# Optimization experiments

Hardware: AMD Instinct MI355X
Metric: run time of the kernel (lower is better)

## Reference

```python
import jax, jax.numpy as jnp
import numpy as np
from jax import lax

INPUT_SIZE = 64
HIDDEN_SIZE = 4096
OUTPUT_SIZE = 16
SEQ_LEN = 4096
SPECTRAL_RADIUS = 0.95
LEAKY_RATE = 0.9
INPUT_SCALING = 1.0
FEEDBACK_SCALING = 0.1
SPARSITY = 0.1


def setup_inputs() -> dict:
    key = jax.random.key(0)
    ks = jax.random.split(key, 7)
    X = jax.random.normal(ks[0], (SEQ_LEN, INPUT_SIZE), dtype=jnp.float32)
    W_in = jax.random.normal(ks[1], (HIDDEN_SIZE, INPUT_SIZE), dtype=jnp.float32) * INPUT_SCALING
    # sparse reservoir matrix, scaled so spectral radius ~ SPECTRAL_RADIUS
    dense = jax.random.normal(ks[2], (HIDDEN_SIZE, HIDDEN_SIZE), dtype=jnp.float32)
    mask = (jax.random.uniform(ks[3], (HIDDEN_SIZE, HIDDEN_SIZE)) < SPARSITY).astype(jnp.float32)
    # circular-law estimate of spectral radius for sparse gaussian: sqrt(density*N)
    scale = SPECTRAL_RADIUS / np.sqrt(SPARSITY * HIDDEN_SIZE)
    W_res = dense * mask * scale
    b = jax.random.normal(ks[4], (HIDDEN_SIZE,), dtype=jnp.float32)
    W_fb = jax.random.normal(ks[5], (HIDDEN_SIZE, OUTPUT_SIZE), dtype=jnp.float32) * FEEDBACK_SCALING
    W_out = jax.random.normal(ks[6], (OUTPUT_SIZE, HIDDEN_SIZE), dtype=jnp.float32) * 0.01
    return {"X": X, "W_in": W_in, "W_res": W_res, "b": b, "W_fb": W_fb, "W_out": W_out}


def reference(X, W_in, W_res, b, W_fb, W_out):
    """ESN with feedback + leaky integration; Force readout (inference: y = W_out @ s).
    Returns (results [T, O], outputs [T, H]) matching ESNForce.forward."""
    H = W_res.shape[0]
    O = W_out.shape[0]

    def step(carry, x_t):
        s, y = carry  # previous state [H], previous output [O]
        pre = W_in @ x_t + W_res @ s + b + W_fb @ y
        s_new = (1.0 - LEAKY_RATE) * s + LEAKY_RATE * jnp.tanh(pre)
        y_new = W_out @ s_new
        return (s_new, y_new), (y_new, s_new)

    init = (jnp.zeros((H,), dtype=X.dtype), jnp.zeros((O,), dtype=X.dtype))
    _, (results, outputs) = lax.scan(step, init, X)
    return results, outputs
```

## Files before the change

### kernel.cpp

```cpp
#include <hip/hip_runtime.h>
#include <cstdint>

#define NBLK 128
#define BLOCK 1024
#define ROWS 32
#define HDIM 4096
#define IDIM 64
#define ODIM 16
#define TSTEPS 4096
#define PAD 576
#define GMAX 18
#define LEAK 0.9f
#define FSTR 16

typedef float f32x4 __attribute__((ext_vector_type(4)));

__global__ void init_ws(unsigned* ws) {
    int i = blockIdx.x * blockDim.x + threadIdx.x;
    if (i < NBLK * FSTR)
        __hip_atomic_store(&ws[i], 0u, __ATOMIC_RELAXED, __HIP_MEMORY_SCOPE_AGENT);
}

__global__ __launch_bounds__(BLOCK) void esn_kernel(
    const float* __restrict__ X,
    const float* __restrict__ Win,
    const float* __restrict__ Wres,
    const float* __restrict__ bvec,
    const float* __restrict__ Wfb,
    const float* __restrict__ Wout,
    float* __restrict__ out,
    float* __restrict__ part,
    unsigned* __restrict__ flags)
{
    __shared__ float          ell_val[ROWS][PAD];
    __shared__ unsigned short ell_idx[ROWS][PAD];
    __shared__ __align__(16) float s_lds[HDIM];
    __shared__ float          win_lds[ROWS][IDIM];
    __shared__ float          wfb_lds[ROWS][ODIM];
    __shared__ __align__(16) float wout_lds[ROWS][ODIM];
    __shared__ float          b_lds[ROWS];
    __shared__ float          x_lds[IDIM];
    __shared__ float          y_lds[ODIM];
    __shared__ __align__(16) float snew_lds[ROWS];
    __shared__ unsigned       prog[NBLK];
    __shared__ int            nnz_lds[ROWS];
    __shared__ int            rnds_lds[ROWS];
    __shared__ unsigned short bankCnt[ROWS][32];
    __shared__ unsigned short grpCnt[ROWS][GMAX];

    const int tid   = threadIdx.x;
    const int blk   = blockIdx.x;
    const int rbase = blk * ROWS;

    for (int i = tid; i < ROWS * PAD; i += BLOCK) {
        ell_val[i / PAD][i % PAD] = 0.0f;
        ell_idx[i / PAD][i % PAD] = 0;
    }
    for (int i = tid; i < ROWS * 32; i += BLOCK) bankCnt[i >> 5][i & 31] = 0;
    for (int i = tid; i < ROWS * GMAX; i += BLOCK) grpCnt[i / GMAX][i % GMAX] = 0;

    {
        const int wave = tid >> 6, lane = tid & 63;
        for (int rr = wave * 2; rr < wave * 2 + 2; ++rr) {
            const float* wrow = Wres + (size_t)(rbase + rr) * HDIM;
            int cnt = 0;
            for (int c0 = 0; c0 < HDIM; c0 += 64)
                cnt += __popcll(__ballot(wrow[c0 + lane] != 0.0f));
            if (lane == 0) {
                int nz = cnt < PAD ? cnt : PAD;
                nnz_lds[rr] = nz;
                int gu = (nz + 31) >> 5;
                if (gu < 1) gu = 1;
                if (gu > GMAX) gu = GMAX;
                rnds_lds[rr] = (gu + 1) >> 1;
            }
        }
    }
    __syncthreads();

    {
        const int wave = tid >> 6, lane = tid & 63;
        if (lane == 0 || lane == 32) {
            const int row = wave * 2 + (lane >> 5);
            const int nz  = nnz_lds[row];
            int gu = (nz + 31) >> 5;
            if (gu < 1) gu = 1;
            if (gu > GMAX) gu = GMAX;
            const float* wrow = Wres + (size_t)(rbase + row) * HDIM;
            int placed = 0;
            for (int c = 0; c < HDIM && placed < nz; ++c) {
                const float w = wrow[c];
                if (w != 0.0f) {
                    const int b = c & 31;
                    const int r = bankCnt[row][b];
                    bankCnt[row][b] = (unsigned short)(r + 1);
                    int g = r % gu;
                    int p = grpCnt[row][g];
                    int guard = 0;
                    while (p >= 32 && guard < GMAX) {
                        g = (g + 1 == gu) ? 0 : g + 1;
                        p = grpCnt[row][g];
                        ++guard;
                    }
                    if (p >= 32) break;
                    grpCnt[row][g] = (unsigned short)(p + 1);
                    const int slot = ((g >> 1) << 6) + 2 * p + (g & 1);
                    ell_val[row][slot] = w;
                    ell_idx[row][slot] = (unsigned short)c;
                    ++placed;
                }
            }
        }
    }

    for (int i = tid; i < ROWS * IDIM; i += BLOCK)
        win_lds[i >> 6][i & 63] = Win[(size_t)(rbase + (i >> 6)) * IDIM + (i & 63)];
    for (int i = tid; i < ROWS * ODIM; i += BLOCK)
        wfb_lds[i >> 4][i & 15] = Wfb[(size_t)(rbase + (i >> 4)) * ODIM + (i & 15)];
    for (int i = tid; i < ROWS * ODIM; i += BLOCK)
        wout_lds[i >> 4][i & 15] = Wout[(size_t)(i & 15) * HDIM + rbase + (i >> 4)];
    if (tid < ROWS) b_lds[tid] = bvec[rbase + tid];

    for (int i = tid; i < HDIM; i += BLOCK) s_lds[i] = 0.0f;
    if (tid < ODIM) y_lds[tid] = 0.0f;
    if (tid >= 64 && tid < 128) x_lds[tid - 64] = X[tid - 64];
    if (tid < NBLK) prog[tid] = 0u;
    __syncthreads();

    float* out_res = out;
    float* out_s   = out + (size_t)TSTEPS * ODIM;

    for (int t = 0; t < TSTEPS; ++t) {
        {
            const int row = tid >> 5;
            const int l   = tid & 31;
            const int R   = rnds_lds[row];
            float a0 = 0.0f, a1 = 0.0f;
            for (int k = 0; k < R; ++k) {
                const int e = (k << 6) + (l << 1);
                const float2  v  = *(const float2*)&ell_val[row][e];
                const ushort2 ix = *(const ushort2*)&ell_idx[row][e];
                a0 += v.x * s_lds[ix.x];
                a1 += v.y * s_lds[ix.y];
            }
            float acc = a0 + a1;
            acc += win_lds[row][l] * x_lds[l] + win_lds[row][l + 32] * x_lds[l + 32];
            if (l < ODIM) acc += wfb_lds[row][l] * y_lds[l];
            acc += __shfl_xor(acc, 16, 32);
            acc += __shfl_xor(acc, 8, 32);
            acc += __shfl_xor(acc, 4, 32);
            acc += __shfl_xor(acc, 2, 32);
            acc += __shfl_xor(acc, 1, 32);
            if (l == 0) {
                const float pre = acc + b_lds[row];
                snew_lds[row] = (1.0f - LEAK) * s_lds[rbase + row] + LEAK * tanhf(pre);
            }
        }
        __syncthreads();

        const int wv = tid >> 6;
        const int ln = tid & 63;
        if (wv == 0) {
            if (ln < ROWS / 4) {
                f32x4 v4 = *(const f32x4*)&snew_lds[ln * 4];
                float* dst = out_s + (size_t)t * HDIM + rbase + ln * 4;
                asm volatile("global_store_dwordx4 %0, %1, off sc0 sc1"
                             :: "v"(dst), "v"(v4) : "memory");
            }
            if (ln < ODIM / 4) {
                f32x4 acc = {0.0f, 0.0f, 0.0f, 0.0f};
                #pragma unroll
                for (int r = 0; r < ROWS; ++r) {
                    f32x4 w = *(const f32x4*)&wout_lds[r][ln * 4];
                    acc += w * snew_lds[r];
                }
                float* dst = part + ((size_t)(t & 1) * NBLK + blk) * ODIM + ln * 4;
                asm volatile("global_store_dwordx4 %0, %1, off sc0 sc1"
                             :: "v"(dst), "v"(acc) : "memory");
            }
            if (ln == 0)
                __hip_atomic_store(&flags[blk * FSTR], (unsigned)(t + 1),
                                   __ATOMIC_RELEASE, __HIP_MEMORY_SCOPE_AGENT);
        } else if (wv == 1) {
            if (t + 1 < TSTEPS) x_lds[ln] = X[(size_t)(t + 1) * IDIM + ln];
            const unsigned tu = (unsigned)(t + 1);
            for (;;) {
                unsigned f0 = __hip_atomic_load(&flags[ln * FSTR],        __ATOMIC_RELAXED, __HIP_MEMORY_SCOPE_AGENT);
                unsigned f1 = __hip_atomic_load(&flags[(ln + 64) * FSTR], __ATOMIC_RELAXED, __HIP_MEMORY_SCOPE_AGENT);
                __hip_atomic_store(&prog[ln],      f0, __ATOMIC_RELAXED, __HIP_MEMORY_SCOPE_WORKGROUP);
                __hip_atomic_store(&prog[ln + 64], f1, __ATOMIC_RELAXED, __HIP_MEMORY_SCOPE_WORKGROUP);
                if (__all(f0 >= tu && f1 >= tu)) break;
                __builtin_amdgcn_s_sleep(1);
            }
            asm volatile("" ::: "memory");
            const int o = ln & 15, j = ln >> 4;
            float* pb = part + (size_t)(t & 1) * NBLK * ODIM;
            float acc = 0.0f;
            #pragma unroll
            for (int k = 0; k < 32; ++k)
                acc += __hip_atomic_load(pb + (size_t)(j + 4 * k) * ODIM + o,
                                         __ATOMIC_RELAXED, __HIP_MEMORY_SCOPE_AGENT);
            acc += __shfl_xor(acc, 16);
            acc += __shfl_xor(acc, 32);
            if (ln < ODIM) {
                if (t + 1 < TSTEPS) y_lds[ln] = acc;
                if (blk == 0) out_res[(size_t)t * ODIM + ln] = acc;
            }
        } else {
            if (t + 1 < TSTEPS) {
                const int wi    = wv - 2;
                const int start = (wi < 2) ? wi * 10 : 20 + (wi - 2) * 9;
                const int count = (wi < 2) ? 10 : 9;
                const unsigned tu = (unsigned)(t + 1);
                for (;;) {
                    unsigned f = (ln < count)
                        ? __hip_atomic_load(&prog[start + ln], __ATOMIC_RELAXED, __HIP_MEMORY_SCOPE_WORKGROUP)
                        : tu;
                    if (__all(f >= tu)) break;
                    __builtin_amdgcn_s_sleep(1);
                }
                asm volatile("" ::: "memory");
                const int c0 = start * ROWS;
                const int n4 = count * (ROWS / 4);
                const float* base = out_s + (size_t)t * HDIM + c0;
                f32x4 v0, v1;
                const float* p0 = base + (size_t)ln * 4;
                asm volatile("global_load_dwordx4 %0, %1, off sc0 sc1"
                             : "=v"(v0) : "v"(p0));
                const bool has2 = (ln + 64) < n4;
                const float* p1 = base + (size_t)(ln + 64) * 4;
                if (has2)
                    asm volatile("global_load_dwordx4 %0, %1, off sc0 sc1"
                                 : "=v"(v1) : "v"(p1));
                asm volatile("s_waitcnt vmcnt(0)" ::: "memory");
                *(f32x4*)&s_lds[c0 + ln * 4] = v0;
                if (has2) *(f32x4*)&s_lds[c0 + (ln + 64) * 4] = v1;
            }
        }
        __syncthreads();
    }
}

extern "C" void kernel_launch(void* const* d_in, const int* in_sizes, int n_in,
                              void* d_out, int out_size, void* d_ws, size_t ws_size,
                              hipStream_t stream) {
    (void)in_sizes; (void)n_in; (void)out_size; (void)ws_size;
    const float* X    = (const float*)d_in[0];
    const float* Win  = (const float*)d_in[1];
    const float* Wres = (const float*)d_in[2];
    const float* b    = (const float*)d_in[3];
    const float* Wfb  = (const float*)d_in[4];
    const float* Wout = (const float*)d_in[5];
    float* out = (float*)d_out;
    unsigned* flags = (unsigned*)d_ws;
    float* part = (float*)d_ws + NBLK * FSTR;

    init_ws<<<8, 256, 0, stream>>>(flags);
    esn_kernel<<<NBLK, BLOCK, 0, stream>>>(X, Win, Wres, b, Wfb, Wout, out, part, flags);
}
```

Before: 21.98 ms.

## Replace flag-based cross-block sync with tagged data packets polled directly

Each 16-byte global store now carries its own step tag, three state values plus a tag or two output partials plus a tag. Consumers poll the data itself until every tag matches, which removes the separate release flag, the LDS progress mirror and the second dependent load round-trip per step. State exchange moves to a double-buffered packed scratch area, and the output partials are split into eight pairs. This relies on 16-byte stores being observed atomically, and busy-polling without sleep raises memory traffic.

```diff
diff --git a/kernel.cpp b/kernel.cpp
--- a/kernel.cpp
+++ b/kernel.cpp
@@ -11,14 +11,15 @@
 #define PAD 576
 #define GMAX 18
 #define LEAK 0.9f
-#define FSTR 16
+#define SU 11
+#define SUS 12
+#define YU 8
 
 typedef float f32x4 __attribute__((ext_vector_type(4)));
 
-__global__ void init_ws(unsigned* ws) {
+__global__ void init_ws(float* ws) {
     int i = blockIdx.x * blockDim.x + threadIdx.x;
-    if (i < NBLK * FSTR)
-        __hip_atomic_store(&ws[i], 0u, __ATOMIC_RELAXED, __HIP_MEMORY_SCOPE_AGENT);
+    if (i < (2 * NBLK * SUS + 2 * NBLK * YU) * 4) ws[i] = 0.0f;
 }
 
 __global__ __launch_bounds__(BLOCK) void esn_kernel(
@@ -29,20 +30,19 @@
     const float* __restrict__ Wfb,
     const float* __restrict__ Wout,
     float* __restrict__ out,
-    float* __restrict__ part,
-    unsigned* __restrict__ flags)
+    float* __restrict__ sx,
+    float* __restrict__ yx)
 {
     __shared__ float          ell_val[ROWS][PAD];
     __shared__ unsigned short ell_idx[ROWS][PAD];
     __shared__ __align__(16) float s_lds[HDIM];
     __shared__ float          win_lds[ROWS][IDIM];
     __shared__ float          wfb_lds[ROWS][ODIM];
-    __shared__ __align__(16) float wout_lds[ROWS][ODIM];
+    __shared__ __align__(8)  float wout_lds[ROWS][ODIM];
     __shared__ float          b_lds[ROWS];
     __shared__ float          x_lds[IDIM];
     __shared__ float          y_lds[ODIM];
     __shared__ __align__(16) float snew_lds[ROWS];
-    __shared__ unsigned       prog[NBLK];
     __shared__ int            nnz_lds[ROWS];
     __shared__ int            rnds_lds[ROWS];
     __shared__ unsigned short bankCnt[ROWS][32];
@@ -124,36 +124,39 @@
     for (int i = tid; i < HDIM; i += BLOCK) s_lds[i] = 0.0f;
     if (tid < ODIM) y_lds[tid] = 0.0f;
     if (tid >= 64 && tid < 128) x_lds[tid - 64] = X[tid - 64];
-    if (tid < NBLK) prog[tid] = 0u;
     __syncthreads();
 
     float* out_res = out;
     float* out_s   = out + (size_t)TSTEPS * ODIM;
 
+    const int rowB = tid >> 5;
+    const int lB   = tid & 31;
+    const int RB   = rnds_lds[rowB];
+
     for (int t = 0; t < TSTEPS; ++t) {
+        const unsigned tu = (unsigned)(t + 1);
+        const float tagf = __uint_as_float(tu);
+
         {
-            const int row = tid >> 5;
-            const int l   = tid & 31;
-            const int R   = rnds_lds[row];
             float a0 = 0.0f, a1 = 0.0f;
-            for (int k = 0; k < R; ++k) {
-                const int e = (k << 6) + (l << 1);
-                const float2  v  = *(const float2*)&ell_val[row][e];
-                const ushort2 ix = *(const ushort2*)&ell_idx[row][e];
+            for (int k = 0; k < RB; ++k) {
+                const int e = (k << 6) + (lB << 1);
+                const float2  v  = *(const float2*)&ell_val[rowB][e];
+                const ushort2 ix = *(const ushort2*)&ell_idx[rowB][e];
                 a0 += v.x * s_lds[ix.x];
                 a1 += v.y * s_lds[ix.y];
             }
             float acc = a0 + a1;
-            acc += win_lds[row][l] * x_lds[l] + win_lds[row][l + 32] * x_lds[l + 32];
-            if (l < ODIM) acc += wfb_lds[row][l] * y_lds[l];
+            acc += win_lds[rowB][lB] * x_lds[lB] + win_lds[rowB][lB + 32] * x_lds[lB + 32];
+            if (lB < ODIM) acc += wfb_lds[rowB][lB] * y_lds[lB];
             acc += __shfl_xor(acc, 16, 32);
             acc += __shfl_xor(acc, 8, 32);
             acc += __shfl_xor(acc, 4, 32);
             acc += __shfl_xor(acc, 2, 32);
             acc += __shfl_xor(acc, 1, 32);
-            if (l == 0) {
-                const float pre = acc + b_lds[row];
-                snew_lds[row] = (1.0f - LEAK) * s_lds[rbase + row] + LEAK * tanhf(pre);
+            if (lB == 0) {
+                const float pre = acc + b_lds[rowB];
+                snew_lds[rowB] = (1.0f - LEAK) * s_lds[rbase + rowB] + LEAK * tanhf(pre);
             }
         }
         __syncthreads();
@@ -161,80 +164,109 @@
         const int wv = tid >> 6;
         const int ln = tid & 63;
         if (wv == 0) {
-            if (ln < ROWS / 4) {
-                f32x4 v4 = *(const f32x4*)&snew_lds[ln * 4];
-                float* dst = out_s + (size_t)t * HDIM + rbase + ln * 4;
+            if (ln >= 16 && ln < 16 + SU) {
+                const int j  = ln - 16;
+                const int b0 = 3 * j;
+                const int b1 = (3 * j + 1 < 32) ? 3 * j + 1 : 31;
+                const int b2 = (3 * j + 2 < 32) ? 3 * j + 2 : 31;
+                f32x4 v;
+                v.x = snew_lds[b0]; v.y = snew_lds[b1]; v.z = snew_lds[b2]; v.w = tagf;
+                float* dst = sx + (((size_t)(t & 1) * NBLK + blk) * SUS + j) * 4;
                 asm volatile("global_store_dwordx4 %0, %1, off sc0 sc1"
-                             :: "v"(dst), "v"(v4) : "memory");
-            }
-            if (ln < ODIM / 4) {
-                f32x4 acc = {0.0f, 0.0f, 0.0f, 0.0f};
+                             :: "v"(dst), "v"(v) : "memory");
+            }
+            if (ln < YU) {
+                float a0 = 0.0f, a1 = 0.0f;
                 #pragma unroll
                 for (int r = 0; r < ROWS; ++r) {
-                    f32x4 w = *(const f32x4*)&wout_lds[r][ln * 4];
-                    acc += w * snew_lds[r];
-                }
-                float* dst = part + ((size_t)(t & 1) * NBLK + blk) * ODIM + ln * 4;
+                    const float2 w = *(const float2*)&wout_lds[r][2 * ln];
+                    a0 += w.x * snew_lds[r];
+                    a1 += w.y * snew_lds[r];
+                }
+                f32x4 v; v.x = a0; v.y = a1; v.z = tagf; v.w = 0.0f;
+                float* dst = yx + (((size_t)(t & 1) * NBLK + blk) * YU + ln) * 4;
                 asm volatile("global_store_dwordx4 %0, %1, off sc0 sc1"
-                             :: "v"(dst), "v"(acc) : "memory");
-            }
-            if (ln == 0)
-                __hip_atomic_store(&flags[blk * FSTR], (unsigned)(t + 1),
-                                   __ATOMIC_RELEASE, __HIP_MEMORY_SCOPE_AGENT);
+                             :: "v"(dst), "v"(v) : "memory");
+            }
+            if (ln >= 32 && ln < 40) {
+                const int j = ln - 32;
+                *(f32x4*)(out_s + (size_t)t * HDIM + rbase + j * 4) =
+                    *(const f32x4*)&snew_lds[j * 4];
+            }
         } else if (wv == 1) {
             if (t + 1 < TSTEPS) x_lds[ln] = X[(size_t)(t + 1) * IDIM + ln];
-            const unsigned tu = (unsigned)(t + 1);
+            const int u  = ln & 7;
+            const int pg = ln >> 3;
+            const float* yb = yx + (size_t)(t & 1) * NBLK * YU * 4;
+            f32x4 w0,w1,w2,w3,w4,w5,w6,w7,w8,w9,w10,w11,w12,w13,w14,w15;
             for (;;) {
-                unsigned f0 = __hip_atomic_load(&flags[ln * FSTR],        __ATOMIC_RELAXED, __HIP_MEMORY_SCOPE_AGENT);
-                unsigned f1 = __hip_atomic_load(&flags[(ln + 64) * FSTR], __ATOMIC_RELAXED, __HIP_MEMORY_SCOPE_AGENT);
-                __hip_atomic_store(&prog[ln],      f0, __ATOMIC_RELAXED, __HIP_MEMORY_SCOPE_WORKGROUP);
-                __hip_atomic_store(&prog[ln + 64], f1, __ATOMIC_RELAXED, __HIP_MEMORY_SCOPE_WORKGROUP);
-                if (__all(f0 >= tu && f1 >= tu)) break;
-                __builtin_amdgcn_s_sleep(1);
-            }
-            asm volatile("" ::: "memory");
-            const int o = ln & 15, j = ln >> 4;
-            float* pb = part + (size_t)(t & 1) * NBLK * ODIM;
-            float acc = 0.0f;
-            #pragma unroll
-            for (int k = 0; k < 32; ++k)
-                acc += __hip_atomic_load(pb + (size_t)(j + 4 * k) * ODIM + o,
-                                         __ATOMIC_RELAXED, __HIP_MEMORY_SCOPE_AGENT);
-            acc += __shfl_xor(acc, 16);
-            acc += __shfl_xor(acc, 32);
-            if (ln < ODIM) {
-                if (t + 1 < TSTEPS) y_lds[ln] = acc;
-                if (blk == 0) out_res[(size_t)t * ODIM + ln] = acc;
+                #define YL(i) asm volatile("global_load_dwordx4 %0, %1, off sc0 sc1" \
+                    : "=v"(w##i) : "v"(yb + (((pg << 4) + i) * YU + u) * 4));
+                YL(0) YL(1) YL(2) YL(3) YL(4) YL(5) YL(6) YL(7)
+                YL(8) YL(9) YL(10) YL(11) YL(12) YL(13) YL(14) YL(15)
+                #undef YL
+                asm volatile("s_waitcnt vmcnt(0)" ::: "memory");
+                __builtin_amdgcn_sched_barrier(0);
+                bool ok = __float_as_uint(w0.z) == tu  && __float_as_uint(w1.z) == tu
+                       && __float_as_uint(w2.z) == tu  && __float_as_uint(w3.z) == tu
+                       && __float_as_uint(w4.z) == tu  && __float_as_uint(w5.z) == tu
+                       && __float_as_uint(w6.z) == tu  && __float_as_uint(w7.z) == tu
+                       && __float_as_uint(w8.z) == tu  && __float_as_uint(w9.z) == tu
+                       && __float_as_uint(w10.z) == tu && __float_as_uint(w11.z) == tu
+                       && __float_as_uint(w12.z) == tu && __float_as_uint(w13.z) == tu
+                       && __float_as_uint(w14.z) == tu && __float_as_uint(w15.z) == tu;
+                if (__all(ok)) break;
+            }
+            float acc0 = ((w0.x + w1.x) + (w2.x + w3.x)) + ((w4.x + w5.x) + (w6.x + w7.x))
+                       + ((w8.x + w9.x) + (w10.x + w11.x)) + ((w12.x + w13.x) + (w14.x + w15.x));
+            float acc1 = ((w0.y + w1.y) + (w2.y + w3.y)) + ((w4.y + w5.y) + (w6.y + w7.y))
+                       + ((w8.y + w9.y) + (w10.y + w11.y)) + ((w12.y + w13.y) + (w14.y + w15.y));
+            acc0 += __shfl_xor(acc0, 8);  acc1 += __shfl_xor(acc1, 8);
+            acc0 += __shfl_xor(acc0, 16); acc1 += __shfl_xor(acc1, 16);
+            acc0 += __shfl_xor(acc0, 32); acc1 += __shfl_xor(acc1, 32);
+            if (ln < 8) {
+                if (t + 1 < TSTEPS) { y_lds[2 * u] = acc0; y_lds[2 * u + 1] = acc1; }
+                if (blk == 0) {
+                    out_res[(size_t)t * ODIM + 2 * u]     = acc0;
+                    out_res[(size_t)t * ODIM + 2 * u + 1] = acc1;
+                }
             }
         } else {
             if (t + 1 < TSTEPS) {
                 const int wi    = wv - 2;
                 const int start = (wi < 2) ? wi * 10 : 20 + (wi - 2) * 9;
                 const int count = (wi < 2) ? 10 : 9;
-                const unsigned tu = (unsigned)(t + 1);
+                const int U     = count * SU;
+                const float* sb = sx + (size_t)(t & 1) * NBLK * SUS * 4;
+                const int g0 = ln, g1 = ln + 64;
+                const int p0 = g0 / SU, u0 = g0 - p0 * SU;
+                const bool h1 = g1 < U;
+                const int p1 = g1 / SU, u1 = g1 - p1 * SU;
+                const float* a0p = sb + (((start + p0) * SUS) + u0) * 4;
+                const float* a1p = sb + (((start + p1) * SUS) + u1) * 4;
+                f32x4 v0, v1;
                 for (;;) {
-                    unsigned f = (ln < count)
-                        ? __hip_atomic_load(&prog[start + ln], __ATOMIC_RELAXED, __HIP_MEMORY_SCOPE_WORKGROUP)
-                        : tu;
-                    if (__all(f >= tu)) break;
-                    __builtin_amdgcn_s_sleep(1);
-                }
-                asm volatile("" ::: "memory");
-                const int c0 = start * ROWS;
-                const int n4 = count * (ROWS / 4);
-                const float* base = out_s + (size_t)t * HDIM + c0;
-                f32x4 v0, v1;
-                const float* p0 = base + (size_t)ln * 4;
-                asm volatile("global_load_dwordx4 %0, %1, off sc0 sc1"
-                             : "=v"(v0) : "v"(p0));
-                const bool has2 = (ln + 64) < n4;
-                const float* p1 = base + (size_t)(ln + 64) * 4;
-                if (has2)
                     asm volatile("global_load_dwordx4 %0, %1, off sc0 sc1"
-                                 : "=v"(v1) : "v"(p1));
-                asm volatile("s_waitcnt vmcnt(0)" ::: "memory");
-                *(f32x4*)&s_lds[c0 + ln * 4] = v0;
-                if (has2) *(f32x4*)&s_lds[c0 + (ln + 64) * 4] = v1;
+                                 : "=v"(v0) : "v"(a0p));
+                    if (h1)
+                        asm volatile("global_load_dwordx4 %0, %1, off sc0 sc1"
+                                     : "=v"(v1) : "v"(a1p));
+                    asm volatile("s_waitcnt vmcnt(0)" ::: "memory");
+                    __builtin_amdgcn_sched_barrier(0);
+                    bool ok = (__float_as_uint(v0.w) == tu) &&
+                              (!h1 || __float_as_uint(v1.w) == tu);
+                    if (__all(ok)) break;
+                }
+                {
+                    const int c0 = (start + p0) * 32 + u0 * 3;
+                    s_lds[c0] = v0.x; s_lds[c0 + 1] = v0.y;
+                    if (u0 != SU - 1) s_lds[c0 + 2] = v0.z;
+                }
+                if (h1) {
+                    const int c1 = (start + p1) * 32 + u1 * 3;
+                    s_lds[c1] = v1.x; s_lds[c1 + 1] = v1.y;
+                    if (u1 != SU - 1) s_lds[c1 + 2] = v1.z;
+                }
             }
         }
         __syncthreads();
@@ -252,9 +284,10 @@
     const float* Wfb  = (const float*)d_in[4];
     const float* Wout = (const float*)d_in[5];
     float* out = (float*)d_out;
-    unsigned* flags = (unsigned*)d_ws;
-    float* part = (float*)d_ws + NBLK * FSTR;
-
-    init_ws<<<8, 256, 0, stream>>>(flags);
-    esn_kernel<<<NBLK, BLOCK, 0, stream>>>(X, Win, Wres, b, Wfb, Wout, out, part, flags);
+    float* sx  = (float*)d_ws;
+    float* yx  = (float*)d_ws + 2 * NBLK * SUS * 4;
+
+    const int words = (2 * NBLK * SUS + 2 * NBLK * YU) * 4;
+    init_ws<<<(words + 255) / 256, 256, 0, stream>>>((float*)d_ws);
+    esn_kernel<<<NBLK, BLOCK, 0, stream>>>(X, Win, Wres, b, Wfb, Wout, out, sx, yx);
 }
```

Result: faster. 20.09 ms (-8.6%).
